# Performance work log

Measured on AMD Instinct MI355X. Metric: run time of the kernel, lower is better.

## Reference

```python
import jax, jax.numpy as jnp
import numpy as np

N = 20000   # nodes
E = 160000  # edges
IN = 16     # in_channels
H = 32      # hidden_channels
MID = 32    # edge-MLP hidden width


def setup_inputs() -> dict:
    key = jax.random.key(0)
    ks = jax.random.split(key, 18)
    s = 0.1  # param scale
    return {
        "x": jax.random.normal(ks[0], (N, IN), jnp.float32),
        "edge_index": jax.random.randint(ks[1], (2, E), 0, N, dtype=jnp.int64),
        "edge_weight": jax.random.uniform(ks[2], (E,), jnp.float32),
        # edge_net1: Linear(1,32) -> SiLU -> Linear(32, IN*H)
        "en1_w1": jax.random.normal(ks[3], (1, MID), jnp.float32) * s,
        "en1_b1": jax.random.normal(ks[4], (MID,), jnp.float32) * s,
        "en1_w2": jax.random.normal(ks[5], (MID, IN * H), jnp.float32) * s,
        "en1_b2": jax.random.normal(ks[6], (IN * H,), jnp.float32) * s,
        "root1": jax.random.normal(ks[7], (IN, H), jnp.float32) * s,
        "bias1": jax.random.normal(ks[8], (H,), jnp.float32) * s,
        # edge_net2: Linear(1,32) -> SiLU -> Linear(32, H*H)
        "en2_w1": jax.random.normal(ks[9], (1, MID), jnp.float32) * s,
        "en2_b1": jax.random.normal(ks[10], (MID,), jnp.float32) * s,
        "en2_w2": jax.random.normal(ks[11], (MID, H * H), jnp.float32) * s,
        "en2_b2": jax.random.normal(ks[12], (H * H,), jnp.float32) * s,
        "root2": jax.random.normal(ks[13], (H, H), jnp.float32) * s,
        "bias2": jax.random.normal(ks[14], (H,), jnp.float32) * s,
        "dec_w": jax.random.normal(ks[15], (H, 1), jnp.float32) * s,
        "dec_b": jax.random.normal(ks[16], (1,), jnp.float32) * s,
    }


def _nnconv(x, src, dst, inv_cnt, e, w1, b1, w2, b2, root, bias, cin, cout):
    # edge MLP -> per-edge [cin, cout] weight matrix
    h = jax.nn.silu(e @ w1 + b1)            # [E, MID]
    w = (h @ w2 + b2).reshape(-1, cin, cout)  # [E, cin, cout]
    msg = jnp.einsum('ei,eio->eo', x[src], w)  # per-edge matmul [E, cout]
    agg = jax.ops.segment_sum(msg, dst, num_segments=N) * inv_cnt  # scatter-mean
    return agg + x @ root + bias


def reference(x, edge_index, edge_weight,
              en1_w1, en1_b1, en1_w2, en1_b2, root1, bias1,
              en2_w1, en2_b1, en2_w2, en2_b2, root2, bias2,
              dec_w, dec_b):
    src, dst = edge_index[0], edge_index[1]
    e = edge_weight[:, None]  # [E, 1]
    cnt = jax.ops.segment_sum(jnp.ones((E,), x.dtype), dst, num_segments=N)
    inv_cnt = (1.0 / jnp.maximum(cnt, 1.0))[:, None]  # [N, 1]
    h = _nnconv(x, src, dst, inv_cnt, e, en1_w1, en1_b1, en1_w2, en1_b2, root1, bias1, IN, H)
    h = jax.nn.silu(h)
    h = _nnconv(h, src, dst, inv_cnt, e, en2_w1, en2_b1, en2_w2, en2_b2, root2, bias2, H, H)
    h = jax.nn.silu(h)
    out = h @ dec_w + dec_b  # [N, 1]
    return out[:, 0]
```

## Files before the change

kernel.cpp:

```cpp
#include <hip/hip_runtime.h>
#include <hip/hip_bf16.h>

#define NN 20000
#define EE 160000
#define HH 32
#define MIDD 32

typedef _Float16 f16x4 __attribute__((ext_vector_type(4)));
typedef _Float16 f16x8 __attribute__((ext_vector_type(8)));
typedef float f32x4 __attribute__((ext_vector_type(4)));

__device__ __forceinline__ float silu_f(float v) {
    return __fdividef(v, 1.0f + __expf(-v));
}

__device__ __forceinline__ void gload_lds_b32(const void* gsrc, void* ldst) {
    __builtin_amdgcn_global_load_lds(
        (const __attribute__((address_space(1))) void*)gsrc,
        (__attribute__((address_space(3))) void*)ldst, 4, 0, 0);
}


__global__ void count_kernel(const int* __restrict__ ei, int* __restrict__ cnt) {
    int e = blockIdx.x * 256 + threadIdx.x;
    if (e < EE) atomicAdd(&cnt[ei[EE + e]], 1);
}

__global__ __launch_bounds__(1024) void scan_kernel(
    const int* __restrict__ cnt, int* __restrict__ off,
    int* __restrict__ cur, float* __restrict__ invc) {
    const int t = threadIdx.x;
    const int base = t * 20;
    __shared__ int wtot[16];

    int c[20];
    if (base + 20 <= NN) {
        const int4* p = (const int4*)(cnt + base);
        #pragma unroll
        for (int q = 0; q < 5; ++q) *(int4*)&c[4 * q] = p[q];
    } else {
        #pragma unroll
        for (int r = 0; r < 20; ++r) {
            int idx = base + r;
            c[r] = (idx < NN) ? cnt[idx] : 0;
        }
    }

    int loc[20];
    int s = 0;
    #pragma unroll
    for (int r = 0; r < 20; ++r) { loc[r] = s; s += c[r]; }

    const int lane = t & 63, wv = t >> 6;
    int incl = s;
    #pragma unroll
    for (int d2 = 1; d2 < 64; d2 <<= 1) {
        int u = __shfl_up(incl, d2);
        if (lane >= d2) incl += u;
    }
    if (lane == 63) wtot[wv] = incl;
    __syncthreads();
    int wbase = 0;
    for (int p2 = 0; p2 < wv; ++p2) wbase += wtot[p2];

    const int excl = wbase + incl - s;

    int o[20];
    #pragma unroll
    for (int r = 0; r < 20; ++r) o[r] = excl + loc[r];
    float iv[20];
    #pragma unroll
    for (int r = 0; r < 20; ++r) iv[r] = 1.0f / fmaxf((float)c[r], 1.0f);

    if (base + 20 <= NN) {
        #pragma unroll
        for (int q = 0; q < 5; ++q) {
            ((int4*)(off + base))[q]    = *(const int4*)&o[4 * q];
            ((int4*)(cur + base))[q]    = *(const int4*)&o[4 * q];
            ((float4*)(invc + base))[q] = *(const float4*)&iv[4 * q];
        }
    } else {
        #pragma unroll
        for (int r = 0; r < 20; ++r) {
            int idx = base + r;
            if (idx < NN) { off[idx] = o[r]; cur[idx] = o[r]; invc[idx] = iv[r]; }
        }
    }
    if (t == 0) off[NN] = EE;
}

__global__ void scatter_kernel(const int* __restrict__ ei, const float* __restrict__ ewt,
                               int* __restrict__ cur, int2* __restrict__ spair) {
    int e = blockIdx.x * 256 + threadIdx.x;
    if (e < EE) {
        int d = ei[EE + e];
        int pos = atomicAdd(&cur[d], 1);
        spair[pos] = make_int2(ei[e], __float_as_int(ewt[e]));
    }
}

__global__ void build_wt(const float* __restrict__ w2a, const float* __restrict__ b2a,
                         const float* __restrict__ ra,
                         const float* __restrict__ w2b, const float* __restrict__ b2b,
                         const float* __restrict__ rb,
                         const float* __restrict__ x,
                         _Float16* __restrict__ Wt1, _Float16* __restrict__ Wt2,
                         _Float16* __restrict__ x16) {
    int idx = blockIdx.x * 256 + threadIdx.x;
    if (idx < 17408) {
        int o = idx / 544, k = idx % 544;
        float v;
        if (k < 512) {
            int m = k & 31, i = k >> 5;
            v = w2a[m * 512 + i * 32 + o];
        } else if (k < 528) {
            v = b2a[(k - 512) * 32 + o];
        } else {
            v = ra[(k - 528) * 32 + o];
        }
        Wt1[o * 544 + k] = (_Float16)v;
    } else if (idx < 52224) {
        int j = idx - 17408;
        int o = j / 1088, k = j % 1088;
        float v;
        if (k < 1024) {
            int m = k & 31, i = k >> 5;
            v = w2b[m * 1024 + i * 32 + o];
        } else if (k < 1056) {
            v = b2b[(k - 1024) * 32 + o];
        } else {
            v = rb[(k - 1056) * 32 + o];
        }
        Wt2[o * 1088 + k] = (_Float16)v;
    } else if (idx < 52224 + NN * 16) {
        int j = idx - 52224;
        x16[j] = (_Float16)x[j];
    }
}


template <int CIN, bool DECODE>
__global__ __launch_bounds__(512, 4) void fused_layer(
    const _Float16* __restrict__ xin16, const int* __restrict__ spair,
    const int* __restrict__ off, const float* __restrict__ invc,
    const float* __restrict__ w1, const float* __restrict__ b1,
    const _Float16* __restrict__ Wt, const float* __restrict__ bias,
    void* __restrict__ outp, const float* __restrict__ dw,
    const float* __restrict__ db) {
    constexpr int K = 34 * CIN;
    constexpr int LDK = K + 4;
    constexpr int steps = K / 32;
    constexpr int CAP = 192;
    constexpr int RPG = 128 / CIN;
    constexpr int LPR = CIN / 2;
    constexpr int NIH = CIN / 16;

    extern __shared__ char smem[];
    _Float16* Fl = (_Float16*)smem;
    char* poolb = smem + (size_t)16 * LDK * 2;
    int* Ps = (int*)poolb;
    _Float16* Xs = (_Float16*)(poolb + (2 * CAP + 64) * 4);
    _Float16* Hs = Xs + CAP * CIN;
    float* red = (float*)poolb;

    const int t = threadIdx.x;
    const int n0 = blockIdx.x * 16;
    const int lane = t & 63, w = t >> 6;
    const int col = lane & 15, g4 = (lane >> 4) * 4;

    const int E0 = off[n0], E1 = off[n0 + 16];
    const int L = E1 - E0;

    const int d0 = n0 + w * 2;
    const int e0l0 = off[d0] - E0;
    const int e1l0 = off[d0 + 1] - E0;
    const int e1l1 = off[d0 + 2] - E0;

    f32x4 aS[2][2][NIH];
    f32x4 a0[2][NIH];
    #pragma unroll
    for (int c = 0; c < 2; ++c) {
        #pragma unroll
        for (int mh = 0; mh < 2; ++mh)
            #pragma unroll
            for (int ih = 0; ih < NIH; ++ih) aS[c][mh][ih] = (f32x4){0.f, 0.f, 0.f, 0.f};
        #pragma unroll
        for (int ih = 0; ih < NIH; ++ih) a0[c][ih] = (f32x4){0.f, 0.f, 0.f, 0.f};
    }

    for (int base = 0; base < L; base += CAP) {
        const int Lc = (L - base < CAP) ? (L - base) : CAP;

        for (int c = w * 64; c < 2 * Lc; c += 512) {
            int gidx = 2 * (E0 + base) + c + lane;
            gidx = (gidx < 2 * EE) ? gidx : (2 * EE - 1);
            gload_lds_b32(spair + gidx, Ps + c);
        }
        __syncthreads();

        {
            const int G = (Lc + RPG - 1) / RPG;
            const int er = lane / LPR, ecp = lane % LPR;
            for (int p = w; p < G; p += 8) {
                int el = p * RPG + er; el = (el < Lc - 1) ? el : (Lc - 1);
                int sn = Ps[2 * el];
                gload_lds_b32(xin16 + (size_t)sn * CIN + 2 * ecp,
                              Xs + (size_t)p * RPG * CIN);
            }
        }
        for (int idx = t; idx < Lc * 32; idx += 512) {
            int e = idx >> 5, m = idx & 31;
            float ew = __int_as_float(Ps[2 * e + 1]);
            Hs[idx] = (_Float16)silu_f(fmaf(ew, w1[m], b1[m]));
        }
        __syncthreads();

        #pragma unroll
        for (int c = 0; c < 2; ++c) {
            int lo = ((c == 0) ? e0l0 : e1l0) - base;
            int hi = ((c == 0) ? e1l0 : e1l1) - base;
            lo = (lo < 0) ? 0 : lo;
            hi = (hi > Lc) ? Lc : hi;
            for (int ks = lo; ks < hi; ks += 32) {
                f16x8 bf[NIH];
                #pragma unroll
                for (int ih = 0; ih < NIH; ++ih)
                    #pragma unroll
                    for (int j = 0; j < 4; ++j) {
                        int k1 = ks + g4 + j, k2 = k1 + 16;
                        int c1 = (k1 < hi) ? k1 : (Lc - 1);
                        int c2 = (k2 < hi) ? k2 : (Lc - 1);
                        bf[ih][j]     = Xs[c1 * CIN + ih * 16 + col];
                        bf[ih][j + 4] = Xs[c2 * CIN + ih * 16 + col];
                    }
                f16x8 af[2];
                #pragma unroll
                for (int mh = 0; mh < 2; ++mh)
                    #pragma unroll
                    for (int j = 0; j < 4; ++j) {
                        int k1 = ks + g4 + j, k2 = k1 + 16;
                        _Float16 v1 = Hs[((k1 < hi) ? k1 : (Lc - 1)) * 32 + mh * 16 + col];
                        _Float16 v2 = Hs[((k2 < hi) ? k2 : (Lc - 1)) * 32 + mh * 16 + col];
                        af[mh][j]     = (k1 < hi) ? v1 : (_Float16)0;
                        af[mh][j + 4] = (k2 < hi) ? v2 : (_Float16)0;
                    }
                f16x8 ao;
                #pragma unroll
                for (int j = 0; j < 4; ++j) {
                    int k1 = ks + g4 + j, k2 = k1 + 16;
                    ao[j]     = (col == 0 && k1 < hi) ? (_Float16)1 : (_Float16)0;
                    ao[j + 4] = (col == 0 && k2 < hi) ? (_Float16)1 : (_Float16)0;
                }
                #pragma unroll
                for (int mh = 0; mh < 2; ++mh)
                    #pragma unroll
                    for (int ih = 0; ih < NIH; ++ih)
                        aS[c][mh][ih] = __builtin_amdgcn_mfma_f32_16x16x32_f16(
                            af[mh], bf[ih], aS[c][mh][ih], 0, 0, 0);
                #pragma unroll
                for (int ih = 0; ih < NIH; ++ih)
                    a0[c][ih] = __builtin_amdgcn_mfma_f32_16x16x32_f16(
                        ao, bf[ih], a0[c][ih], 0, 0, 0);
            }
        }
        if (base + CAP < L) __syncthreads();
    }

    #pragma unroll
    for (int c = 0; c < 2; ++c) {
        const int d = n0 + w * 2 + c;
        const float iv = invc[d];
        _Float16* Fr = Fl + (size_t)(w * 2 + c) * LDK;
        #pragma unroll
        for (int mh = 0; mh < 2; ++mh)
            #pragma unroll
            for (int ih = 0; ih < NIH; ++ih)
                #pragma unroll
                for (int r = 0; r < 4; ++r)
                    Fr[32 * (ih * 16 + col) + mh * 16 + g4 + r] =
                        (_Float16)(aS[c][mh][ih][r] * iv);
        if (g4 == 0) {
            #pragma unroll
            for (int ih = 0; ih < NIH; ++ih)
                Fr[32 * CIN + ih * 16 + col] = (_Float16)(a0[c][ih][0] * iv);
        }
        if (lane >= CIN && lane < 2 * CIN)
            Fr[32 * CIN + lane] = xin16[(size_t)d * CIN + (lane - CIN)];
    }
    __syncthreads();

    const int o16 = col, g = lane >> 4;

    const _Float16* Arow = Fl + (size_t)o16 * LDK + g * 4;
    const _Float16* B0 = Wt + (size_t)o16 * K + g * 4;
    const _Float16* B1 = Wt + (size_t)(o16 + 16) * K + g * 4;

    f32x4 acc0 = {0.f, 0.f, 0.f, 0.f};
    f32x4 acc1 = {0.f, 0.f, 0.f, 0.f};

    const int sb = (steps * w) >> 3;
    const int se = (steps * (w + 1)) >> 3;
    #pragma unroll 2
    for (int s = sb; s < se; ++s) {
        const int k0 = s * 32;
        f16x4 alo = *(const f16x4*)(Arow + k0);
        f16x4 ahi = *(const f16x4*)(Arow + k0 + 16);
        f16x4 b0l = *(const f16x4*)(B0 + k0);
        f16x4 b0h = *(const f16x4*)(B0 + k0 + 16);
        f16x4 b1l = *(const f16x4*)(B1 + k0);
        f16x4 b1h = *(const f16x4*)(B1 + k0 + 16);
        f16x8 a, bb0, bb1;
        #pragma unroll
        for (int j = 0; j < 4; ++j) {
            a[j] = alo[j];  a[j + 4] = ahi[j];
            bb0[j] = b0l[j]; bb0[j + 4] = b0h[j];
            bb1[j] = b1l[j]; bb1[j + 4] = b1h[j];
        }
        acc0 = __builtin_amdgcn_mfma_f32_16x16x32_f16(a, bb0, acc0, 0, 0, 0);
        acc1 = __builtin_amdgcn_mfma_f32_16x16x32_f16(a, bb1, acc1, 0, 0, 0);
    }

    if (w > 0) {
        float* rw = red + (w - 1) * 512;
        #pragma unroll
        for (int r = 0; r < 4; ++r) {
            rw[(g * 4 + r) * 32 + o16]      = acc0[r];
            rw[(g * 4 + r) * 32 + 16 + o16] = acc1[r];
        }
    }
    __syncthreads();
    if (w == 0) {
        #pragma unroll
        for (int r = 0; r < 4; ++r) {
            const int ro = (g * 4 + r) * 32 + o16;
            #pragma unroll
            for (int p = 0; p < 7; ++p) {
                acc0[r] += red[p * 512 + ro];
                acc1[r] += red[p * 512 + ro + 16];
            }
        }
        const float bb0 = bias[o16], bb1 = bias[o16 + 16];
        const int nrow = n0 + g * 4;
        if (!DECODE) {
            _Float16* op = (_Float16*)outp;
            #pragma unroll
            for (int r = 0; r < 4; ++r) {
                op[(size_t)(nrow + r) * 32 + o16]      = (_Float16)silu_f(acc0[r] + bb0);
                op[(size_t)(nrow + r) * 32 + 16 + o16] = (_Float16)silu_f(acc1[r] + bb1);
            }
        } else {
            float* op = (float*)outp;
            const float w0 = dw[o16], w1v = dw[o16 + 16];
            const float dbv = db[0];
            #pragma unroll
            for (int r = 0; r < 4; ++r) {
                float p = silu_f(acc0[r] + bb0) * w0 + silu_f(acc1[r] + bb1) * w1v;
                p += __shfl_xor(p, 1);
                p += __shfl_xor(p, 2);
                p += __shfl_xor(p, 4);
                p += __shfl_xor(p, 8);
                if (o16 == 0) op[nrow + r] = p + dbv;
            }
        }
    }
}


extern "C" void kernel_launch(void* const* d_in, const int* in_sizes, int n_in,
                              void* d_out, int out_size, void* d_ws, size_t ws_size,
                              hipStream_t stream) {
    const float* x      = (const float*)d_in[0];
    const int*   ei     = (const int*)d_in[1];
    const float* ew     = (const float*)d_in[2];
    const float* en1_w1 = (const float*)d_in[3];
    const float* en1_b1 = (const float*)d_in[4];
    const float* en1_w2 = (const float*)d_in[5];
    const float* en1_b2 = (const float*)d_in[6];
    const float* root1  = (const float*)d_in[7];
    const float* bias1  = (const float*)d_in[8];
    const float* en2_w1 = (const float*)d_in[9];
    const float* en2_b1 = (const float*)d_in[10];
    const float* en2_w2 = (const float*)d_in[11];
    const float* en2_b2 = (const float*)d_in[12];
    const float* root2  = (const float*)d_in[13];
    const float* bias2  = (const float*)d_in[14];
    const float* dec_w  = (const float*)d_in[15];
    const float* dec_b  = (const float*)d_in[16];
    float* out = (float*)d_out;
    (void)in_sizes; (void)n_in; (void)out_size; (void)ws_size;

    char* wp = (char*)d_ws;
    auto alloc = [&](size_t bytes) {
        char* p = wp;
        wp += (bytes + 255) & ~(size_t)255;
        return p;
    };
    int*      cnt   = (int*)alloc((size_t)NN * 4);
    int*      off   = (int*)alloc((size_t)(NN + 1) * 4);
    int*      cur   = (int*)alloc((size_t)NN * 4);
    float*    invc  = (float*)alloc((size_t)NN * 4);
    int2*     spair = (int2*)alloc((size_t)EE * 8);
    _Float16* h1h   = (_Float16*)alloc((size_t)NN * 32 * 2);
    _Float16* x16   = (_Float16*)alloc((size_t)NN * 16 * 2);
    _Float16* Wt1   = (_Float16*)alloc((size_t)17408 * 2);
    _Float16* Wt2   = (_Float16*)alloc((size_t)34816 * 2);

    hipMemsetAsync(cnt, 0, (size_t)NN * 4, stream);

    count_kernel<<<(EE + 255) / 256, 256, 0, stream>>>(ei, cnt);
    scan_kernel<<<1, 1024, 0, stream>>>(cnt, off, cur, invc);
    scatter_kernel<<<(EE + 255) / 256, 256, 0, stream>>>(ei, ew, cur, spair);
    build_wt<<<(52224 + NN * 16 + 255) / 256, 256, 0, stream>>>(
        en1_w2, en1_b2, root1, en2_w2, en2_b2, root2, x, Wt1, Wt2, x16);

    auto f1 = fused_layer<16, false>;
    auto f2 = fused_layer<32, true>;
    (void)hipFuncSetAttribute((const void*)f1,
                              hipFuncAttributeMaxDynamicSharedMemorySize, 163840);
    (void)hipFuncSetAttribute((const void*)f2,
                              hipFuncAttributeMaxDynamicSharedMemorySize, 163840);

    const size_t lds1 = (size_t)16 * (34 * 16 + 4) * 2 + (448 * 4 + 192 * 16 * 2 + 192 * 64);
    const size_t lds2 = (size_t)16 * (34 * 32 + 4) * 2 + (448 * 4 + 192 * 32 * 2 + 192 * 64);

    fused_layer<16, false><<<NN / 16, 512, lds1, stream>>>(
        x16, (const int*)spair, off, invc, en1_w1, en1_b1, Wt1, bias1, h1h,
        nullptr, nullptr);
    fused_layer<32, true><<<NN / 16, 512, lds2, stream>>>(
        h1h, (const int*)spair, off, invc, en2_w1, en2_b1, Wt2, bias2, out,
        dec_w, dec_b);
}
```

Baseline: 99.57 us.

## Replace global-atomic CSR build with per-block LDS histograms and deterministic scatter

Builds the destination-sorted edge list with 128 blocks, each counting its edges into a packed 16-bit LDS histogram. A column scan over the block histograms gives per-block offsets, and a second pass places edges using LDS atomic ranks instead of global atomics on a cursor array. The histogram work is fused into the weight-building kernel and the memset is removed, aiming to cut global atomic contention and launch count. In exchange it adds an extra kernel and a 10 MB histogram buffer that is written, column-scanned and read again.

```diff
diff --git a/kernel.cpp b/kernel.cpp
--- a/kernel.cpp
+++ b/kernel.cpp
@@ -5,6 +5,8 @@
 #define EE 160000
 #define HH 32
 #define MIDD 32
+#define NB 128
+#define EPB 1250
 
 typedef _Float16 f16x4 __attribute__((ext_vector_type(4)));
 typedef _Float16 f16x8 __attribute__((ext_vector_type(8)));
@@ -20,93 +22,33 @@
         (__attribute__((address_space(3))) void*)ldst, 4, 0, 0);
 }
 
-
-__global__ void count_kernel(const int* __restrict__ ei, int* __restrict__ cnt) {
-    int e = blockIdx.x * 256 + threadIdx.x;
-    if (e < EE) atomicAdd(&cnt[ei[EE + e]], 1);
-}
-
-__global__ __launch_bounds__(1024) void scan_kernel(
-    const int* __restrict__ cnt, int* __restrict__ off,
-    int* __restrict__ cur, float* __restrict__ invc) {
+__global__ __launch_bounds__(256) void prep_kernel(
+    const int* __restrict__ ei,
+    const float* __restrict__ w2a, const float* __restrict__ b2a,
+    const float* __restrict__ ra,
+    const float* __restrict__ w2b, const float* __restrict__ b2b,
+    const float* __restrict__ rb,
+    const float* __restrict__ x,
+    unsigned int* __restrict__ histG,
+    _Float16* __restrict__ Wt1, _Float16* __restrict__ Wt2,
+    _Float16* __restrict__ x16) {
     const int t = threadIdx.x;
-    const int base = t * 20;
-    __shared__ int wtot[16];
-
-    int c[20];
-    if (base + 20 <= NN) {
-        const int4* p = (const int4*)(cnt + base);
-        #pragma unroll
-        for (int q = 0; q < 5; ++q) *(int4*)&c[4 * q] = p[q];
-    } else {
-        #pragma unroll
-        for (int r = 0; r < 20; ++r) {
-            int idx = base + r;
-            c[r] = (idx < NN) ? cnt[idx] : 0;
-        }
-    }
-
-    int loc[20];
-    int s = 0;
-    #pragma unroll
-    for (int r = 0; r < 20; ++r) { loc[r] = s; s += c[r]; }
-
-    const int lane = t & 63, wv = t >> 6;
-    int incl = s;
-    #pragma unroll
-    for (int d2 = 1; d2 < 64; d2 <<= 1) {
-        int u = __shfl_up(incl, d2);
-        if (lane >= d2) incl += u;
-    }
-    if (lane == 63) wtot[wv] = incl;
-    __syncthreads();
-    int wbase = 0;
-    for (int p2 = 0; p2 < wv; ++p2) wbase += wtot[p2];
-
-    const int excl = wbase + incl - s;
-
-    int o[20];
-    #pragma unroll
-    for (int r = 0; r < 20; ++r) o[r] = excl + loc[r];
-    float iv[20];
-    #pragma unroll
-    for (int r = 0; r < 20; ++r) iv[r] = 1.0f / fmaxf((float)c[r], 1.0f);
-
-    if (base + 20 <= NN) {
-        #pragma unroll
-        for (int q = 0; q < 5; ++q) {
-            ((int4*)(off + base))[q]    = *(const int4*)&o[4 * q];
-            ((int4*)(cur + base))[q]    = *(const int4*)&o[4 * q];
-            ((float4*)(invc + base))[q] = *(const float4*)&iv[4 * q];
-        }
-    } else {
-        #pragma unroll
-        for (int r = 0; r < 20; ++r) {
-            int idx = base + r;
-            if (idx < NN) { off[idx] = o[r]; cur[idx] = o[r]; invc[idx] = iv[r]; }
-        }
-    }
-    if (t == 0) off[NN] = EE;
-}
-
-__global__ void scatter_kernel(const int* __restrict__ ei, const float* __restrict__ ewt,
-                               int* __restrict__ cur, int2* __restrict__ spair) {
-    int e = blockIdx.x * 256 + threadIdx.x;
-    if (e < EE) {
-        int d = ei[EE + e];
-        int pos = atomicAdd(&cur[d], 1);
-        spair[pos] = make_int2(ei[e], __float_as_int(ewt[e]));
-    }
-}
-
-__global__ void build_wt(const float* __restrict__ w2a, const float* __restrict__ b2a,
-                         const float* __restrict__ ra,
-                         const float* __restrict__ w2b, const float* __restrict__ b2b,
-                         const float* __restrict__ rb,
-                         const float* __restrict__ x,
-                         _Float16* __restrict__ Wt1, _Float16* __restrict__ Wt2,
-                         _Float16* __restrict__ x16) {
-    int idx = blockIdx.x * 256 + threadIdx.x;
+    if (blockIdx.x < NB) {
+        __shared__ unsigned int h2[NN / 2];
+        for (int i = t; i < NN / 2; i += 256) h2[i] = 0u;
+        __syncthreads();
+        const int base = blockIdx.x * EPB;
+        for (int e = base + t; e < base + EPB; e += 256) {
+            int d = ei[EE + e];
+            atomicAdd(&h2[d >> 1], 1u << ((d & 1) * 16));
+        }
+        __syncthreads();
+        unsigned int* outp = histG + (size_t)blockIdx.x * NN;
+        for (int n = t; n < NN; n += 256)
+            outp[n] = (h2[n >> 1] >> ((n & 1) * 16)) & 0xFFFFu;
+        return;
+    }
+    int idx = (blockIdx.x - NB) * 256 + t;
     if (idx < 17408) {
         int o = idx / 544, k = idx % 544;
         float v;
@@ -135,6 +77,97 @@
     } else if (idx < 52224 + NN * 16) {
         int j = idx - 52224;
         x16[j] = (_Float16)x[j];
+    }
+}
+
+__global__ __launch_bounds__(256) void colscan_kernel(
+    unsigned int* __restrict__ histG, int* __restrict__ cnt,
+    float* __restrict__ invc) {
+    const int n = blockIdx.x * 256 + threadIdx.x;
+    if (n >= NN) return;
+    unsigned int s = 0;
+    #pragma unroll 4
+    for (int b = 0; b < NB; ++b) {
+        unsigned int v = histG[(size_t)b * NN + n];
+        histG[(size_t)b * NN + n] = s;
+        s += v;
+    }
+    cnt[n] = (int)s;
+    invc[n] = 1.0f / fmaxf((float)s, 1.0f);
+}
+
+__global__ __launch_bounds__(1024) void scan_kernel(
+    const int* __restrict__ cnt, int* __restrict__ off) {
+    const int t = threadIdx.x;
+    const int base = t * 20;
+    __shared__ int wtot[16];
+
+    int c[20];
+    if (base + 20 <= NN) {
+        const int4* p = (const int4*)(cnt + base);
+        #pragma unroll
+        for (int q = 0; q < 5; ++q) *(int4*)&c[4 * q] = p[q];
+    } else {
+        #pragma unroll
+        for (int r = 0; r < 20; ++r) {
+            int idx = base + r;
+            c[r] = (idx < NN) ? cnt[idx] : 0;
+        }
+    }
+
+    int loc[20];
+    int s = 0;
+    #pragma unroll
+    for (int r = 0; r < 20; ++r) { loc[r] = s; s += c[r]; }
+
+    const int lane = t & 63, wv = t >> 6;
+    int incl = s;
+    #pragma unroll
+    for (int d2 = 1; d2 < 64; d2 <<= 1) {
+        int u = __shfl_up(incl, d2);
+        if (lane >= d2) incl += u;
+    }
+    if (lane == 63) wtot[wv] = incl;
+    __syncthreads();
+    int wbase = 0;
+    for (int p2 = 0; p2 < wv; ++p2) wbase += wtot[p2];
+
+    const int excl = wbase + incl - s;
+
+    int o[20];
+    #pragma unroll
+    for (int r = 0; r < 20; ++r) o[r] = excl + loc[r];
+
+    if (base + 20 <= NN) {
+        #pragma unroll
+        for (int q = 0; q < 5; ++q)
+            ((int4*)(off + base))[q] = *(const int4*)&o[4 * q];
+    } else {
+        #pragma unroll
+        for (int r = 0; r < 20; ++r) {
+            int idx = base + r;
+            if (idx < NN) off[idx] = o[r];
+        }
+    }
+    if (t == 0) off[NN] = EE;
+}
+
+__global__ __launch_bounds__(256) void scatter2_kernel(
+    const int* __restrict__ ei, const float* __restrict__ ewt,
+    const int* __restrict__ off, const unsigned int* __restrict__ histG,
+    int2* __restrict__ spair) {
+    __shared__ unsigned int r2[NN / 2];
+    const int t = threadIdx.x, b = blockIdx.x;
+    for (int i = t; i < NN / 2; i += 256) r2[i] = 0u;
+    __syncthreads();
+    const int base = b * EPB;
+    const unsigned int* hb = histG + (size_t)b * NN;
+    for (int e = base + t; e < base + EPB; e += 256) {
+        int d = ei[EE + e];
+        unsigned int old = atomicAdd(&r2[d >> 1], 1u << ((d & 1) * 16));
+        int rank = (int)((old >> ((d & 1) * 16)) & 0xFFFFu);
+        int pos = off[d] + (int)hb[d] + rank;
+        spair[pos] = make_int2(ei[e], __float_as_int(ewt[e]));
     }
 }
 
@@ -395,9 +428,9 @@
         wp += (bytes + 255) & ~(size_t)255;
         return p;
     };
+    unsigned int* histG = (unsigned int*)alloc((size_t)NB * NN * 4);
     int*      cnt   = (int*)alloc((size_t)NN * 4);
     int*      off   = (int*)alloc((size_t)(NN + 1) * 4);
-    int*      cur   = (int*)alloc((size_t)NN * 4);
     float*    invc  = (float*)alloc((size_t)NN * 4);
     int2*     spair = (int2*)alloc((size_t)EE * 8);
     _Float16* h1h   = (_Float16*)alloc((size_t)NN * 32 * 2);
@@ -405,13 +438,13 @@
     _Float16* Wt1   = (_Float16*)alloc((size_t)17408 * 2);
     _Float16* Wt2   = (_Float16*)alloc((size_t)34816 * 2);
 
-    hipMemsetAsync(cnt, 0, (size_t)NN * 4, stream);
-
-    count_kernel<<<(EE + 255) / 256, 256, 0, stream>>>(ei, cnt);
-    scan_kernel<<<1, 1024, 0, stream>>>(cnt, off, cur, invc);
-    scatter_kernel<<<(EE + 255) / 256, 256, 0, stream>>>(ei, ew, cur, spair);
-    build_wt<<<(52224 + NN * 16 + 255) / 256, 256, 0, stream>>>(
-        en1_w2, en1_b2, root1, en2_w2, en2_b2, root2, x, Wt1, Wt2, x16);
+    const int build_blocks = (52224 + NN * 16 + 255) / 256;
+    prep_kernel<<<NB + build_blocks, 256, 0, stream>>>(
+        ei, en1_w2, en1_b2, root1, en2_w2, en2_b2, root2, x,
+        histG, Wt1, Wt2, x16);
+    colscan_kernel<<<(NN + 255) / 256, 256, 0, stream>>>(histG, cnt, invc);
+    scan_kernel<<<1, 1024, 0, stream>>>(cnt, off);
+    scatter2_kernel<<<NB, 256, 0, stream>>>(ei, ew, off, histG, spair);
 
     auto f1 = fused_layer<16, false>;
     auto f2 = fused_layer<32, true>;
```

New measurement: 97.23 us. -2.4%, faster.
